# Performance work log

Measured on AMD Instinct MI355X. Metric: run time of the kernel, lower is better.

The kernel has to match this reference:

```python
import jax, jax.numpy as jnp
import numpy as np

TOP_K = 2

def setup_inputs() -> dict:
    key = jax.random.key(0)
    k1, k2 = jax.random.split(key)
    hidden_states = jax.random.normal(k1, (16384, 4096), dtype=jnp.float32)
    W = jax.random.normal(k2, (64, 4096), dtype=jnp.float32) * 0.02  # classifier weight [num_experts, hidden]
    return {"hidden_states": hidden_states, "W": W}

def reference(hidden_states, W):
    # router logits: [T, E]
    router_logits = jnp.einsum('th,eh->te', hidden_states, W)
    # softmax in float32 (matches dtype=torch.float)
    router_probs = jax.nn.softmax(router_logits.astype(jnp.float32), axis=-1)
    # top-k over experts, then renormalize selected weights
    topk_weight, topk_experts_index = jax.lax.top_k(router_probs, TOP_K)
    topk_weight = topk_weight / jnp.sum(topk_weight, axis=-1, keepdims=True)
    return (topk_weight, router_logits, topk_experts_index)
```

## Files before the change

kernel.cpp:

```cpp
#include <hip/hip_runtime.h>

constexpr int T  = 16384;
constexpr int HD = 4096;
constexpr int E  = 64;
constexpr int BK = 32;
constexpr int NCH = HD / BK;

using short8 = __attribute__((ext_vector_type(8))) short;
using f32x4  = __attribute__((ext_vector_type(4))) float;

#define AS1 __attribute__((address_space(1)))
#define AS3 __attribute__((address_space(3)))

__device__ __forceinline__ unsigned short f2bf(float x) {
  union { float f; unsigned u; } v; v.f = x;
  return (unsigned short)((v.u + 0x7FFFu + ((v.u >> 16) & 1u)) >> 16);
}
__device__ __forceinline__ float bf2f(unsigned short h) {
  union { float f; unsigned u; } v; v.u = ((unsigned)h) << 16;
  return v.f;
}

__device__ __forceinline__ void gload16(const void* g, void* l) {
  __builtin_amdgcn_global_load_lds((const AS1 void*)g, (AS3 void*)l, 16, 0, 0);
}

__global__ __launch_bounds__(256) void wprep(const float* __restrict__ W,
                                             short* __restrict__ img) {
  const int tid = blockIdx.x * 256 + threadIdx.x;
  const int c   = tid >> 9;
  const int rem = tid & 511;
  const int e   = rem >> 3;
  const int sp  = rem & 7;
  const int s   = sp ^ (e & 7);
  const int part = s >> 2;
  const int sl  = s & 3;
  const float* src = W + (size_t)e * HD + c * BK + sl * 8;
  short8 v;
#pragma unroll
  for (int j = 0; j < 8; ++j) {
    float x = src[j];
    unsigned short h = f2bf(x);
    v[j] = part ? (short)f2bf(x - bf2f(h)) : (short)h;
  }
  *(short8*)(img + (size_t)tid * 8) = v;
}

__global__ __launch_bounds__(256) void router_gemm(const float* __restrict__ H,
                                                   const short* __restrict__ wsB,
                                                   float* __restrict__ logits) {
  __shared__ __align__(16) char lds_raw[3 * 8192 + 2 * 8192];

  const int tid  = threadIdx.x;
  const int w    = tid >> 6;
  const int lane = tid & 63;
  const int q    = lane >> 4;
  const int r    = lane & 15;
  const int row0 = blockIdx.x * 64;

  f32x4 acc[4];
#pragma unroll
  for (int ct = 0; ct < 4; ++ct)
#pragma unroll
    for (int i = 0; i < 4; ++i) acc[ct][i] = 0.f;

  auto stageA = [&](int chunk, int abuf) {
    char* dst = lds_raw + abuf * 8192 + w * 2048;
#pragma unroll
    for (int j = 0; j < 2; ++j) {
      const int rl = 8 * j + (lane >> 3);
      const int R  = 16 * w + rl;
      const int s  = (lane & 7) ^ (R & 7);
      const char* src = (const char*)H + ((size_t)(row0 + R) * HD + chunk * BK) * 4 + s * 16;
      gload16(src, dst + j * 1024);
    }
  };
  auto stageB = [&](int chunk, int bbuf) {
    char* dst = lds_raw + 24576 + bbuf * 8192 + w * 2048;
    const char* src = (const char*)wsB + (size_t)chunk * 8192 + w * 2048 + lane * 16;
    gload16(src, dst);
    gload16(src + 1024, dst + 1024);
  };

  const int Rrow = 16 * w + r;
  const int ra   = Rrow & 7;

  auto compute = [&](int abuf, int bbuf) {
    const char* Ar = lds_raw + abuf * 8192 + Rrow * 128;
    const char* Bb = lds_raw + 24576 + bbuf * 8192;
    f32x4 a0 = *(const f32x4*)(Ar + ((2 * q) ^ ra) * 16);
    f32x4 a1 = *(const f32x4*)(Ar + ((2 * q + 1) ^ ra) * 16);
    short8 ahi, alo;
#pragma unroll
    for (int jj = 0; jj < 4; ++jj) {
      unsigned short h0 = f2bf(a0[jj]);
      ahi[jj] = (short)h0; alo[jj] = (short)f2bf(a0[jj] - bf2f(h0));
      unsigned short h1 = f2bf(a1[jj]);
      ahi[4 + jj] = (short)h1; alo[4 + jj] = (short)f2bf(a1[jj] - bf2f(h1));
    }
#pragma unroll
    for (int ct = 0; ct < 4; ++ct) {
      const int e = 16 * ct + r;
      const char* Br = Bb + e * 128;
      short8 bhi = *(const short8*)(Br + ((q) ^ (e & 7)) * 16);
      short8 blo = *(const short8*)(Br + ((4 + q) ^ (e & 7)) * 16);
      acc[ct] = __builtin_amdgcn_mfma_f32_16x16x32_bf16(ahi, bhi, acc[ct], 0, 0, 0);
      acc[ct] = __builtin_amdgcn_mfma_f32_16x16x32_bf16(alo, bhi, acc[ct], 0, 0, 0);
      acc[ct] = __builtin_amdgcn_mfma_f32_16x16x32_bf16(ahi, blo, acc[ct], 0, 0, 0);
    }
  };

  stageA(0, 0);
  stageB(0, 0);
  stageA(1, 1);

  int ab = 0, bb = 0;
  for (int t = 0; t < NCH - 2; ++t) {
    asm volatile("s_waitcnt vmcnt(2)\n\ts_barrier" ::: "memory");
    stageB(t + 1, bb ^ 1);
    int ab2 = ab + 2; if (ab2 >= 3) ab2 -= 3;
    stageA(t + 2, ab2);
    compute(ab, bb);
    ab = (ab == 2) ? 0 : ab + 1;
    bb ^= 1;
  }
  asm volatile("s_waitcnt vmcnt(2)\n\ts_barrier" ::: "memory");
  stageB(NCH - 1, bb ^ 1);
  compute(ab, bb);
  ab = (ab == 2) ? 0 : ab + 1;
  bb ^= 1;
  asm volatile("s_waitcnt vmcnt(0)\n\ts_barrier" ::: "memory");
  compute(ab, bb);

  const int orow = row0 + 16 * w + 4 * q;
#pragma unroll
  for (int ct = 0; ct < 4; ++ct)
#pragma unroll
    for (int rr = 0; rr < 4; ++rr)
      logits[(size_t)(orow + rr) * E + 16 * ct + r] = acc[ct][rr];
}

__global__ __launch_bounds__(256) void router_topk(const float* __restrict__ logits,
                                                   float* __restrict__ topw,
                                                   float* __restrict__ topi) {
  const int tid  = threadIdx.x;
  const int lane = tid & 63;
  const int row  = blockIdx.x * 4 + (tid >> 6);

  const float x = logits[(size_t)row * E + lane];

  float m = x;
#pragma unroll
  for (int off = 32; off; off >>= 1) m = fmaxf(m, __shfl_xor(m, off));
  const float p = expf(x - m);
  float s = p;
#pragma unroll
  for (int off = 32; off; off >>= 1) s += __shfl_xor(s, off);
  const float prob = p / s;

  float v1 = prob; int i1 = lane;
#pragma unroll
  for (int off = 32; off; off >>= 1) {
    const float ov = __shfl_xor(v1, off);
    const int   oi = __shfl_xor(i1, off);
    if (ov > v1 || (ov == v1 && oi < i1)) { v1 = ov; i1 = oi; }
  }
  float v2 = (lane == i1) ? -1.0f : prob; int i2 = lane;
#pragma unroll
  for (int off = 32; off; off >>= 1) {
    const float ov = __shfl_xor(v2, off);
    const int   oi = __shfl_xor(i2, off);
    if (ov > v2 || (ov == v2 && oi < i2)) { v2 = ov; i2 = oi; }
  }

  if (lane == 0) {
    const float sum = v1 + v2;
    topw[(size_t)row * 2 + 0] = v1 / sum;
    topw[(size_t)row * 2 + 1] = v2 / sum;
    topi[(size_t)row * 2 + 0] = (float)i1;
    topi[(size_t)row * 2 + 1] = (float)i2;
  }
}

extern "C" void kernel_launch(void* const* d_in, const int* in_sizes, int n_in,
                              void* d_out, int out_size, void* d_ws, size_t ws_size,
                              hipStream_t stream) {
  const float* H = (const float*)d_in[0];
  const float* W = (const float*)d_in[1];

  float* out    = (float*)d_out;
  float* topw   = out;
  float* logits = out + (size_t)T * 2;
  float* topi   = logits + (size_t)T * E;

  short* wimg = (short*)d_ws;

  wprep<<<256, 256, 0, stream>>>(W, wimg);
  router_gemm<<<T / 64, 256, 0, stream>>>(H, wimg, logits);
  router_topk<<<T / 4, 256, 0, stream>>>(logits, topw, topi);
}
```

Measured before the change: 83.59 us.

## Fuse top-k into router GEMM and retile to 32-row blocks with 64-wide K chunks

Removes the separate softmax/top-k kernel. Top-2 is now computed directly on the logits inside the GEMM epilogue, using shuffles and an LDS candidate merge, and the renormalized weights come from a sigmoid of the logit difference. The GEMM is retiled: 32 rows per block, 512 threads, each wave computing one 16x16 tile, and BK raised to 64 with a matching weight-image layout. This saves a launch and the logits re-read, and the smaller row tiles create more blocks to hide latency. The cost is more LDS per block and a different per-wave compute balance.

After: 87.80 us. 5.0% more time.

```diff
diff --git a/kernel.cpp b/kernel.cpp
--- a/kernel.cpp
+++ b/kernel.cpp
@@ -1,10 +1,11 @@
 #include <hip/hip_runtime.h>
 
-constexpr int T  = 16384;
-constexpr int HD = 4096;
-constexpr int E  = 64;
-constexpr int BK = 32;
+constexpr int T   = 16384;
+constexpr int HD  = 4096;
+constexpr int E   = 64;
+constexpr int BK  = 64;
 constexpr int NCH = HD / BK;
+constexpr int BM  = 32;
 
 using short8 = __attribute__((ext_vector_type(8))) short;
 using f32x4  = __attribute__((ext_vector_type(4))) float;
@@ -28,14 +29,12 @@
 __global__ __launch_bounds__(256) void wprep(const float* __restrict__ W,
                                              short* __restrict__ img) {
   const int tid = blockIdx.x * 256 + threadIdx.x;
-  const int c   = tid >> 9;
-  const int rem = tid & 511;
-  const int e   = rem >> 3;
-  const int sp  = rem & 7;
-  const int s   = sp ^ (e & 7);
-  const int part = s >> 2;
-  const int sl  = s & 3;
-  const float* src = W + (size_t)e * HD + c * BK + sl * 8;
+  const int c    = tid >> 10;
+  const int e    = (tid >> 4) & 63;
+  const int sp   = tid & 15;
+  const int part = sp >> 3;
+  const int g    = (sp & 7) ^ (e & 7);
+  const float* src = W + (size_t)e * HD + c * BK + g * 8;
   short8 v;
 #pragma unroll
   for (int j = 0; j < 8; ++j) {
@@ -46,67 +45,69 @@
   *(short8*)(img + (size_t)tid * 8) = v;
 }
 
-__global__ __launch_bounds__(256) void router_gemm(const float* __restrict__ H,
-                                                   const short* __restrict__ wsB,
-                                                   float* __restrict__ logits) {
-  __shared__ __align__(16) char lds_raw[3 * 8192 + 2 * 8192];
+__global__ __launch_bounds__(512, 4) void router_gemm(
+    const float* __restrict__ H, const short* __restrict__ img,
+    float* __restrict__ logits, float* __restrict__ topw, float* __restrict__ topi) {
+  __shared__ __align__(16) char lds[59392];
+  char* const ldsA = lds;
+  char* const ldsB = lds + 24576;
+  float* const cand = (float*)(lds + 57344);
 
   const int tid  = threadIdx.x;
   const int w    = tid >> 6;
   const int lane = tid & 63;
   const int q    = lane >> 4;
   const int r    = lane & 15;
-  const int row0 = blockIdx.x * 64;
-
-  f32x4 acc[4];
-#pragma unroll
-  for (int ct = 0; ct < 4; ++ct)
-#pragma unroll
-    for (int i = 0; i < 4; ++i) acc[ct][i] = 0.f;
-
-  auto stageA = [&](int chunk, int abuf) {
-    char* dst = lds_raw + abuf * 8192 + w * 2048;
-#pragma unroll
-    for (int j = 0; j < 2; ++j) {
-      const int rl = 8 * j + (lane >> 3);
-      const int R  = 16 * w + rl;
-      const int s  = (lane & 7) ^ (R & 7);
-      const char* src = (const char*)H + ((size_t)(row0 + R) * HD + chunk * BK) * 4 + s * 16;
-      gload16(src, dst + j * 1024);
-    }
+  const int rt   = w >> 2;
+  const int ct   = w & 3;
+  const int row0 = blockIdx.x * BM;
+
+  f32x4 acc = {0.f, 0.f, 0.f, 0.f};
+
+  auto stageA = [&](int c, int buf) {
+    const int R  = tid >> 4;
+    const int sp = tid & 15;
+    const int s  = (sp & 8) | ((sp & 7) ^ (R & 7));
+    const char* src = (const char*)(H + (size_t)(row0 + R) * HD + c * BK) + s * 16;
+    gload16(src, ldsA + buf * 8192 + w * 1024);
   };
-  auto stageB = [&](int chunk, int bbuf) {
-    char* dst = lds_raw + 24576 + bbuf * 8192 + w * 2048;
-    const char* src = (const char*)wsB + (size_t)chunk * 8192 + w * 2048 + lane * 16;
-    gload16(src, dst);
-    gload16(src + 1024, dst + 1024);
+  auto stageB = [&](int c, int buf) {
+    const char* srcb = (const char*)img + (size_t)c * 16384;
+    char* dstb = ldsB + buf * 16384;
+#pragma unroll
+    for (int j = 0; j < 2; ++j)
+      gload16(srcb + (size_t)(j * 512 + tid) * 16, dstb + (j * 512 + w * 64) * 16);
   };
 
-  const int Rrow = 16 * w + r;
-  const int ra   = Rrow & 7;
+  const int Arow = 16 * rt + r;
+  const int ra   = r & 7;
 
   auto compute = [&](int abuf, int bbuf) {
-    const char* Ar = lds_raw + abuf * 8192 + Rrow * 128;
-    const char* Bb = lds_raw + 24576 + bbuf * 8192;
-    f32x4 a0 = *(const f32x4*)(Ar + ((2 * q) ^ ra) * 16);
-    f32x4 a1 = *(const f32x4*)(Ar + ((2 * q + 1) ^ ra) * 16);
-    short8 ahi, alo;
-#pragma unroll
-    for (int jj = 0; jj < 4; ++jj) {
-      unsigned short h0 = f2bf(a0[jj]);
-      ahi[jj] = (short)h0; alo[jj] = (short)f2bf(a0[jj] - bf2f(h0));
-      unsigned short h1 = f2bf(a1[jj]);
-      ahi[4 + jj] = (short)h1; alo[4 + jj] = (short)f2bf(a1[jj] - bf2f(h1));
-    }
-#pragma unroll
-    for (int ct = 0; ct < 4; ++ct) {
-      const int e = 16 * ct + r;
-      const char* Br = Bb + e * 128;
-      short8 bhi = *(const short8*)(Br + ((q) ^ (e & 7)) * 16);
-      short8 blo = *(const short8*)(Br + ((4 + q) ^ (e & 7)) * 16);
-      acc[ct] = __builtin_amdgcn_mfma_f32_16x16x32_bf16(ahi, bhi, acc[ct], 0, 0, 0);
-      acc[ct] = __builtin_amdgcn_mfma_f32_16x16x32_bf16(alo, bhi, acc[ct], 0, 0, 0);
-      acc[ct] = __builtin_amdgcn_mfma_f32_16x16x32_bf16(ahi, blo, acc[ct], 0, 0, 0);
+    const char* Ab = ldsA + abuf * 8192 + Arow * 256;
+    const char* Bb = ldsB + bbuf * 16384 + (16 * ct + r) * 256;
+#pragma unroll
+    for (int kk = 0; kk < 2; ++kk) {
+      const int s0  = 8 * kk + 2 * q;
+      const int sp0 = (s0 & 8) | ((s0 & 7) ^ ra);
+      const int s1  = s0 + 1;
+      const int sp1 = (s1 & 8) | ((s1 & 7) ^ ra);
+      f32x4 a0 = *(const f32x4*)(Ab + sp0 * 16);
+      f32x4 a1 = *(const f32x4*)(Ab + sp1 * 16);
+      const int gh  = 4 * kk + q;
+      const int sph = gh ^ ra;
+      short8 bh = *(const short8*)(Bb + sph * 16);
+      short8 bl = *(const short8*)(Bb + (8 | sph) * 16);
+      short8 ahi, alo;
+#pragma unroll
+      for (int j = 0; j < 4; ++j) {
+        unsigned short h0 = f2bf(a0[j]);
+        ahi[j] = (short)h0; alo[j] = (short)f2bf(a0[j] - bf2f(h0));
+        unsigned short h1 = f2bf(a1[j]);
+        ahi[4 + j] = (short)h1; alo[4 + j] = (short)f2bf(a1[j] - bf2f(h1));
+      }
+      acc = __builtin_amdgcn_mfma_f32_16x16x32_bf16(ahi, bh, acc, 0, 0, 0);
+      acc = __builtin_amdgcn_mfma_f32_16x16x32_bf16(alo, bh, acc, 0, 0, 0);
+      acc = __builtin_amdgcn_mfma_f32_16x16x32_bf16(ahi, bl, acc, 0, 0, 0);
     }
   };
 
@@ -116,7 +117,7 @@
 
   int ab = 0, bb = 0;
   for (int t = 0; t < NCH - 2; ++t) {
-    asm volatile("s_waitcnt vmcnt(2)\n\ts_barrier" ::: "memory");
+    asm volatile("s_waitcnt vmcnt(1)\n\ts_barrier" ::: "memory");
     stageB(t + 1, bb ^ 1);
     int ab2 = ab + 2; if (ab2 >= 3) ab2 -= 3;
     stageA(t + 2, ab2);
@@ -124,7 +125,7 @@
     ab = (ab == 2) ? 0 : ab + 1;
     bb ^= 1;
   }
-  asm volatile("s_waitcnt vmcnt(2)\n\ts_barrier" ::: "memory");
+  asm volatile("s_waitcnt vmcnt(1)\n\ts_barrier" ::: "memory");
   stageB(NCH - 1, bb ^ 1);
   compute(ab, bb);
   ab = (ab == 2) ? 0 : ab + 1;
@@ -132,53 +133,53 @@
   asm volatile("s_waitcnt vmcnt(0)\n\ts_barrier" ::: "memory");
   compute(ab, bb);
 
-  const int orow = row0 + 16 * w + 4 * q;
-#pragma unroll
-  for (int ct = 0; ct < 4; ++ct)
-#pragma unroll
-    for (int rr = 0; rr < 4; ++rr)
-      logits[(size_t)(orow + rr) * E + 16 * ct + r] = acc[ct][rr];
-}
-
-__global__ __launch_bounds__(256) void router_topk(const float* __restrict__ logits,
-                                                   float* __restrict__ topw,
-                                                   float* __restrict__ topi) {
-  const int tid  = threadIdx.x;
-  const int lane = tid & 63;
-  const int row  = blockIdx.x * 4 + (tid >> 6);
-
-  const float x = logits[(size_t)row * E + lane];
-
-  float m = x;
-#pragma unroll
-  for (int off = 32; off; off >>= 1) m = fmaxf(m, __shfl_xor(m, off));
-  const float p = expf(x - m);
-  float s = p;
-#pragma unroll
-  for (int off = 32; off; off >>= 1) s += __shfl_xor(s, off);
-  const float prob = p / s;
-
-  float v1 = prob; int i1 = lane;
-#pragma unroll
-  for (int off = 32; off; off >>= 1) {
-    const float ov = __shfl_xor(v1, off);
-    const int   oi = __shfl_xor(i1, off);
-    if (ov > v1 || (ov == v1 && oi < i1)) { v1 = ov; i1 = oi; }
-  }
-  float v2 = (lane == i1) ? -1.0f : prob; int i2 = lane;
-#pragma unroll
-  for (int off = 32; off; off >>= 1) {
-    const float ov = __shfl_xor(v2, off);
-    const int   oi = __shfl_xor(i2, off);
-    if (ov > v2 || (ov == v2 && oi < i2)) { v2 = ov; i2 = oi; }
-  }
-
-  if (lane == 0) {
-    const float sum = v1 + v2;
-    topw[(size_t)row * 2 + 0] = v1 / sum;
-    topw[(size_t)row * 2 + 1] = v2 / sum;
-    topi[(size_t)row * 2 + 0] = (float)i1;
-    topi[(size_t)row * 2 + 1] = (float)i2;
+  const int orow0 = row0 + 16 * rt + 4 * q;
+#pragma unroll
+  for (int rr = 0; rr < 4; ++rr)
+    logits[(size_t)(orow0 + rr) * E + 16 * ct + r] = acc[rr];
+
+#pragma unroll
+  for (int rr = 0; rr < 4; ++rr) {
+    const int myi = 16 * ct + r;
+    float v1 = acc[rr]; int i1 = myi;
+#pragma unroll
+    for (int off = 1; off < 16; off <<= 1) {
+      float ov = __shfl_xor(v1, off); int oi = __shfl_xor(i1, off);
+      if (ov > v1 || (ov == v1 && oi < i1)) { v1 = ov; i1 = oi; }
+    }
+    float v2 = (myi == i1) ? -3.4e38f : acc[rr]; int i2 = myi;
+#pragma unroll
+    for (int off = 1; off < 16; off <<= 1) {
+      float ov = __shfl_xor(v2, off); int oi = __shfl_xor(i2, off);
+      if (ov > v2 || (ov == v2 && oi < i2)) { v2 = ov; i2 = oi; }
+    }
+    if (r == 0) {
+      float* cd = cand + ((size_t)(16 * rt + 4 * q + rr) * 4 + ct) * 4;
+      cd[0] = v1; cd[1] = (float)i1; cd[2] = v2; cd[3] = (float)i2;
+    }
+  }
+  __syncthreads();
+
+  if (tid < BM) {
+    const float* cd = cand + (size_t)tid * 16;
+    float bv = -3.4e38f; int bi = 1 << 30;
+#pragma unroll
+    for (int j = 0; j < 8; ++j) {
+      float v = cd[2 * j]; int i = (int)cd[2 * j + 1];
+      if (v > bv || (v == bv && i < bi)) { bv = v; bi = i; }
+    }
+    float sv = -3.4e38f; int si = 1 << 30;
+#pragma unroll
+    for (int j = 0; j < 8; ++j) {
+      float v = cd[2 * j]; int i = (int)cd[2 * j + 1];
+      if (i != bi && (v > sv || (v == sv && i < si))) { sv = v; si = i; }
+    }
+    const float w1 = 1.0f / (1.0f + __expf(sv - bv));
+    const int R = row0 + tid;
+    topw[(size_t)R * 2 + 0] = w1;
+    topw[(size_t)R * 2 + 1] = 1.0f - w1;
+    topi[(size_t)R * 2 + 0] = (float)bi;
+    topi[(size_t)R * 2 + 1] = (float)si;
   }
 }
 
@@ -196,6 +197,5 @@
   short* wimg = (short*)d_ws;
 
   wprep<<<256, 256, 0, stream>>>(W, wimg);
-  router_gemm<<<T / 64, 256, 0, stream>>>(H, wimg, logits);
-  router_topk<<<T / 4, 256, 0, stream>>>(logits, topw, topi);
-}
+  router_gemm<<<T / BM, 512, 0, stream>>>(H, wimg, logits, topw, topi);
+}
```
